# Performance work log

Hardware: AMD Instinct MI355X
Metric: run time of the kernel (lower is better)

The kernel has to match this reference:

```python
import jax, jax.numpy as jnp
import numpy as np

NUM_NODES = 50000
NUM_EDGES = 400000
NUM_GRAPHS = 16


def _glorot(key, shape):
    fan_in, fan_out = shape[0], shape[1]
    lim = jnp.sqrt(6.0 / (fan_in + fan_out))
    return jax.random.uniform(key, shape, jnp.float32, -lim, lim)


def setup_inputs() -> dict:
    key = jax.random.key(0)
    ks = jax.random.split(key, 12)
    x = jax.random.normal(ks[0], (NUM_NODES, 3), jnp.float32)
    edge_index = jax.random.randint(ks[1], (2, NUM_EDGES), 0, NUM_NODES, jnp.int64)
    batch = jax.random.randint(ks[2], (NUM_NODES,), 0, NUM_GRAPHS, jnp.int64)
    return {
        "x": x,
        "edge_index": edge_index,
        "batch": batch,
        "W1": _glorot(ks[3], (3, 512)),   "b1": jnp.zeros((512,), jnp.float32),
        "W2": _glorot(ks[4], (512, 1024)), "b2": jnp.zeros((1024,), jnp.float32),
        "W3": _glorot(ks[5], (1024, 512)), "b3": jnp.zeros((512,), jnp.float32),
        "fcw1": _glorot(ks[6], (512, 128)), "fcb1": jnp.zeros((128,), jnp.float32),
        "fcw2": _glorot(ks[7], (128, 1)),   "fcb2": jnp.zeros((1,), jnp.float32),
    }


def _gcn_conv(x, W, b, row, col, n):
    # PyG GCNConv: h = x W; out_i = sum_{j->i} d_j^{-1/2} d_i^{-1/2} h_j + b
    # (row, col) already include self-loops; edge weights are 1.
    h = x @ W  # [N, out]
    deg = jnp.zeros((n,), h.dtype).at[col].add(1.0)  # in-degree incl. self-loop
    dis = jax.lax.rsqrt(deg)  # deg >= 1 thanks to self-loops
    norm = dis[row] * dis[col]  # [E]
    msgs = h[row] * norm[:, None]  # [E, out] gather
    return jax.ops.segment_sum(msgs, col, num_segments=n) + b


def reference(x, edge_index, batch, W1, b1, W2, b2, W3, b3, fcw1, fcb1, fcw2, fcb2):
    n = x.shape[0]
    loop = jnp.arange(n, dtype=edge_index.dtype)
    row = jnp.concatenate([edge_index[0], loop])  # source
    col = jnp.concatenate([edge_index[1], loop])  # target

    h = jax.nn.relu(_gcn_conv(x, W1, b1, row, col, n))
    h = jax.nn.relu(_gcn_conv(h, W2, b2, row, col, n))
    h = jax.nn.relu(_gcn_conv(h, W3, b3, row, col, n))

    # global mean pool over graphs in the batch
    sums = jax.ops.segment_sum(h, batch, num_segments=NUM_GRAPHS)  # [G, 512]
    cnts = jax.ops.segment_sum(jnp.ones((n,), h.dtype), batch, num_segments=NUM_GRAPHS)
    pooled = sums / jnp.maximum(cnts, 1.0)[:, None]

    out = jax.nn.relu(pooled @ fcw1 + fcb1)
    out = out @ fcw2 + fcb2  # [G, 1]
    return out
```

## Files before the change

kernel.cpp:

```cpp
#include <hip/hip_runtime.h>
#include <hip/hip_bf16.h>

#define NNODES 50000
#define NEDGES 400000
#define NGRAPH 16

typedef __attribute__((ext_vector_type(4))) float floatx4;
typedef __attribute__((ext_vector_type(8))) short short8;

typedef __attribute__((address_space(3))) unsigned int lds_uint;
typedef __attribute__((address_space(1))) const unsigned int gbl_uint;

__device__ __forceinline__ void load16_to_lds(const void* g, void* l) {
    __builtin_amdgcn_global_load_lds((gbl_uint*)g, (lds_uint*)l, 16, 0, 0);
}

__global__ __launch_bounds__(64) void zero_out_k(float* out, int n) {
    int i = blockIdx.x * 64 + threadIdx.x;
    if (i < n) out[i] = 0.0f;
}

__global__ __launch_bounds__(256) void init_k(int* deg_cnt, int* cursor,
                                              float* gsum, int* gcnt,
                                              const float* __restrict__ x,
                                              float4* __restrict__ xp, int n) {
    int i = blockIdx.x * 256 + threadIdx.x;
    if (i < n) {
        deg_cnt[i] = 0; cursor[i] = 0;
        xp[i] = make_float4(x[i * 3 + 0], x[i * 3 + 1], x[i * 3 + 2], 0.0f);
    }
    if (i < NGRAPH * 512) gsum[i] = 0.0f;
    if (i < NGRAPH) gcnt[i] = 0;
}

__global__ __launch_bounds__(256) void deg_k(const int* __restrict__ col,
                                             int* __restrict__ deg_cnt, int e) {
    int i = blockIdx.x * 256 + threadIdx.x;
    if (i < e) atomicAdd(&deg_cnt[col[i]], 1);
}

__global__ __launch_bounds__(256) void segsum_k(const int* __restrict__ cnt,
                                                int* __restrict__ segsum, int n) {
    __shared__ int sb[256];
    int seg = blockIdx.x;
    int base = seg * 1024;
    int t = threadIdx.x;
    int s = 0;
#pragma unroll
    for (int j = 0; j < 4; ++j) {
        int idx = base + t + j * 256;
        if (idx < n) s += cnt[idx];
    }
    sb[t] = s;
    __syncthreads();
    for (int off = 128; off > 0; off >>= 1) {
        if (t < off) sb[t] += sb[t + off];
        __syncthreads();
    }
    if (t == 0) segsum[seg] = sb[0];
}

__global__ __launch_bounds__(64) void segscan_k(const int* __restrict__ segsum,
                                                int* __restrict__ segbase,
                                                int* __restrict__ offs,
                                                int nseg, int n) {
    if (threadIdx.x == 0) {
        int run = 0;
        for (int s = 0; s < nseg; ++s) { segbase[s] = run; run += segsum[s]; }
        offs[n] = run;
    }
}

__global__ __launch_bounds__(1024) void offs_k(const int* __restrict__ cnt,
                                               const int* __restrict__ segbase,
                                               int* __restrict__ offs,
                                               float* __restrict__ dis, int n) {
    __shared__ int sb[1024];
    int seg = blockIdx.x;
    int t = threadIdx.x;
    int i = seg * 1024 + t;
    int c = (i < n) ? cnt[i] : 0;
    sb[t] = c;
    __syncthreads();
    for (int off = 1; off < 1024; off <<= 1) {
        int v = (t >= off) ? sb[t - off] : 0;
        __syncthreads();
        sb[t] += v;
        __syncthreads();
    }
    if (i < n) {
        offs[i] = segbase[seg] + sb[t] - c;
        dis[i]  = rsqrtf((float)(c + 1));
    }
}

__global__ __launch_bounds__(256) void scatter_k(const int* __restrict__ row,
                                                 const int* __restrict__ col,
                                                 const int* __restrict__ offs,
                                                 int* __restrict__ cursor,
                                                 int* __restrict__ ssrc,
                                                 float* __restrict__ sw,
                                                 const float* __restrict__ dis, int e) {
    int i = blockIdx.x * 256 + threadIdx.x;
    if (i >= e) return;
    int d = col[i];
    int p = offs[d] + atomicAdd(&cursor[d], 1);
    int s = row[i];
    ssrc[p] = s;
    sw[p]   = dis[s];
}

__global__ __launch_bounds__(256) void agg3_k(const float4* __restrict__ xp,
                                              float* __restrict__ out,
                                              const int* __restrict__ offs,
                                              const int* __restrict__ ssrc,
                                              const float* __restrict__ sw,
                                              const float* __restrict__ dis, int n) {
    int d = blockIdx.x * 256 + threadIdx.x;
    if (d >= n) return;
    float dd = dis[d];
    float4 xd = xp[d];
    float a0 = dd * xd.x, a1 = dd * xd.y, a2 = dd * xd.z;
    int beg = offs[d], end = offs[d + 1];
    for (int e = beg; e < end; ++e) {
        int s = ssrc[e];
        float w = sw[e];
        float4 q = xp[s];
        a0 += w * q.x; a1 += w * q.y; a2 += w * q.z;
    }
    out[d * 3 + 0] = dd * a0;
    out[d * 3 + 1] = dd * a1;
    out[d * 3 + 2] = dd * a2;
}

__global__ __launch_bounds__(256) void gemm1_k(const float* __restrict__ aggx,
                                               const float* __restrict__ W1,
                                               const float* __restrict__ b1,
                                               __hip_bfloat16* __restrict__ h1, int n) {
    int wave = threadIdx.x >> 6;
    int lane = threadIdx.x & 63;
    int d = blockIdx.x * 4 + wave;
    if (d >= n) return;
    float a0 = aggx[d * 3 + 0], a1 = aggx[d * 3 + 1], a2 = aggx[d * 3 + 2];
    int f0 = lane * 8;
    short8 ov;
#pragma unroll
    for (int j = 0; j < 8; ++j) {
        int f = f0 + j;
        float v = b1[f] + a0 * W1[f] + a1 * W1[512 + f] + a2 * W1[1024 + f];
        __hip_bfloat16 h = __float2bfloat16(fmaxf(v, 0.0f));
        ov[j] = *(short*)&h;
    }
    *(short8*)&h1[(size_t)d * 512 + f0] = ov;
}

__device__ inline float bs2f(short v) {
    return __uint_as_float(((unsigned int)(unsigned short)v) << 16);
}

__global__ __launch_bounds__(256) void agg512w_k(const __hip_bfloat16* __restrict__ in,
                                                 __hip_bfloat16* __restrict__ out,
                                                 const int* __restrict__ offs,
                                                 const int* __restrict__ ssrc,
                                                 const float* __restrict__ sw,
                                                 const float* __restrict__ dis,
                                                 const float* __restrict__ bias,
                                                 int relu, int n) {
    int wave = threadIdx.x >> 6;
    int lane = threadIdx.x & 63;
    int d = blockIdx.x * 4 + wave;
    if (d >= n) return;
    float dd = dis[d];
    short8 p = *(const short8*)&in[(size_t)d * 512 + lane * 8];
    float acc[8];
#pragma unroll
    for (int j = 0; j < 8; ++j) acc[j] = dd * bs2f(p[j]);

    int beg = offs[d], end = offs[d + 1];
    int e = beg;
    for (; e + 3 < end; e += 4) {
        int s0 = ssrc[e],     s1 = ssrc[e + 1];
        int s2 = ssrc[e + 2], s3 = ssrc[e + 3];
        float w0 = sw[e],     w1 = sw[e + 1];
        float w2 = sw[e + 2], w3 = sw[e + 3];
        short8 q0 = *(const short8*)&in[(size_t)s0 * 512 + lane * 8];
        short8 q1 = *(const short8*)&in[(size_t)s1 * 512 + lane * 8];
        short8 q2 = *(const short8*)&in[(size_t)s2 * 512 + lane * 8];
        short8 q3 = *(const short8*)&in[(size_t)s3 * 512 + lane * 8];
#pragma unroll
        for (int j = 0; j < 8; ++j) acc[j] += w0 * bs2f(q0[j]);
#pragma unroll
        for (int j = 0; j < 8; ++j) acc[j] += w1 * bs2f(q1[j]);
#pragma unroll
        for (int j = 0; j < 8; ++j) acc[j] += w2 * bs2f(q2[j]);
#pragma unroll
        for (int j = 0; j < 8; ++j) acc[j] += w3 * bs2f(q3[j]);
    }
    for (; e < end; ++e) {
        int s0 = ssrc[e];
        float w0 = sw[e];
        short8 q0 = *(const short8*)&in[(size_t)s0 * 512 + lane * 8];
#pragma unroll
        for (int j = 0; j < 8; ++j) acc[j] += w0 * bs2f(q0[j]);
    }

    short8 ov;
#pragma unroll
    for (int j = 0; j < 8; ++j) {
        float v = acc[j] * dd;
        if (bias) v += bias[lane * 8 + j];
        if (relu) v = fmaxf(v, 0.0f);
        __hip_bfloat16 h = __float2bfloat16(v);
        ov[j] = *(short*)&h;
    }
    *(short8*)&out[(size_t)d * 512 + lane * 8] = ov;
}

__global__ __launch_bounds__(256) void tcvt_k(const float* __restrict__ W2,
                                              __hip_bfloat16* __restrict__ w2t,
                                              const float* __restrict__ W3,
                                              __hip_bfloat16* __restrict__ w3t) {
    __shared__ float tile[32][33];
    int t = threadIdx.x;
    const float* W; __hip_bfloat16* Wt;
    int K, N, idx;
    if (blockIdx.x < 512) { W = W2; Wt = w2t; K = 512;  N = 1024; idx = blockIdx.x; }
    else                  { W = W3; Wt = w3t; K = 1024; N = 512;  idx = blockIdx.x - 512; }
    int nbn = N / 32;
    int bn = (idx % nbn) * 32;
    int bk = (idx / nbn) * 32;
    int c = t & 31, r0 = t >> 5;
#pragma unroll
    for (int j = 0; j < 4; ++j) {
        int r = r0 + j * 8;
        tile[r][c] = W[(size_t)(bk + r) * N + bn + c];
    }
    __syncthreads();
#pragma unroll
    for (int j = 0; j < 4; ++j) {
        int r = r0 + j * 8;
        Wt[(size_t)(bn + r) * K + bk + c] = __float2bfloat16(tile[c][r]);
    }
}

__global__ __launch_bounds__(512, 2) void mfma_gemm256_k(
        const __hip_bfloat16* __restrict__ A,
        const __hip_bfloat16* __restrict__ Bt,
        const float* __restrict__ bias,
        __hip_bfloat16* __restrict__ C,
        int M, int N, int K, int relu, int lnt) {
    __shared__ short smem[65536];

    int tid  = threadIdx.x;
    int lane = tid & 63;
    int wave = tid >> 6;
    int wm = wave >> 2;
    int wn = wave & 3;
    int fr = lane & 15;

    int nwg = gridDim.x;
    int wg  = (blockIdx.x & 7) * (nwg >> 3) + (blockIdx.x >> 3);
    int mt  = wg >> lnt;
    int nt  = wg & ((1 << lnt) - 1);
    int bm  = mt << 8;
    int bn  = nt << 8;

    int r = lane & 15;
    int s = lane >> 4;
    const __hip_bfloat16* ga[2];
    const __hip_bfloat16* gb[2];
#pragma unroll
    for (int j = 0; j < 2; ++j) {
        int gsub = 2 * wave + j;
        ga[j] = A  + (size_t)(bm + gsub * 16 + r) * K + s * 8;
        gb[j] = Bt + (size_t)(bn + gsub * 16 + r) * K + s * 8;
    }

    floatx4 acc[8][4] = {};

    auto stage = [&](int p) {
        short* sp = &smem[p * 16384];
#pragma unroll
        for (int j = 0; j < 2; ++j) {
            load16_to_lds(ga[j], sp + (2 * wave + j) * 512);
            load16_to_lds(gb[j], sp + 8192 + (2 * wave + j) * 512);
            ga[j] += 32;
            gb[j] += 32;
        }
    };

    auto compute = [&](int p) {
        const short* sm = &smem[p * 16384];
        short8 bfr[4];
#pragma unroll
        for (int ni = 0; ni < 4; ++ni)
            bfr[ni] = *(const short8*)&sm[8192 + (wn * 4 + ni) * 512 + lane * 8];
#pragma unroll
        for (int mh = 0; mh < 2; ++mh) {
            short8 afr[4];
#pragma unroll
            for (int mi = 0; mi < 4; ++mi)
                afr[mi] = *(const short8*)&sm[(wm * 8 + mh * 4 + mi) * 512 + lane * 8];
            __builtin_amdgcn_s_setprio(1);
#pragma unroll
            for (int mi = 0; mi < 4; ++mi)
#pragma unroll
                for (int ni = 0; ni < 4; ++ni)
                    acc[mh * 4 + mi][ni] = __builtin_amdgcn_mfma_f32_16x16x32_bf16(
                        afr[mi], bfr[ni], acc[mh * 4 + mi][ni], 0, 0, 0);
            __builtin_amdgcn_s_setprio(0);
        }
    };

    int KT = K >> 5;
    stage(0); stage(1); stage(2);
    for (int t = 0; t < KT - 3; ++t) {
        stage((t + 3) & 3);
        asm volatile("s_waitcnt vmcnt(12)" ::: "memory");
        __builtin_amdgcn_s_barrier();
        compute(t & 3);
        __builtin_amdgcn_s_barrier();
    }
    asm volatile("s_waitcnt vmcnt(8)" ::: "memory");
    __builtin_amdgcn_s_barrier();
    compute((KT - 3) & 3);
    asm volatile("s_waitcnt vmcnt(4)" ::: "memory");
    __builtin_amdgcn_s_barrier();
    compute((KT - 2) & 3);
    asm volatile("s_waitcnt vmcnt(0)" ::: "memory");
    __builtin_amdgcn_s_barrier();
    compute((KT - 1) & 3);

    short* Cs = smem;
    int l4 = lane >> 4;
#pragma unroll
    for (int h = 0; h < 2; ++h) {
        __builtin_amdgcn_s_barrier();
        if (wm == h) {
#pragma unroll
            for (int mi = 0; mi < 8; ++mi) {
#pragma unroll
                for (int ni = 0; ni < 4; ++ni) {
                    int rr = mi * 16 + l4 * 4;
                    int cc = wn * 64 + ni * 16 + fr;
                    float bv = bias ? bias[bn + cc] : 0.0f;
#pragma unroll
                    for (int q = 0; q < 4; ++q) {
                        float v = acc[mi][ni][q] + bv;
                        if (relu) v = fmaxf(v, 0.0f);
                        __hip_bfloat16 hh = __float2bfloat16(v);
                        Cs[(rr + q) * 264 + cc] = *(short*)&hh;
                    }
                }
            }
        }
        __builtin_amdgcn_s_barrier();
#pragma unroll
        for (int i = 0; i < 8; ++i) {
            int idx = tid + 512 * i;
            int rr = idx >> 5, cc = idx & 31;
            int grow = bm + h * 128 + rr;
            if (grow < M)
                *(short8*)&C[(size_t)grow * N + bn + cc * 8] =
                    *(const short8*)&Cs[rr * 264 + cc * 8];
        }
    }
}

__global__ __launch_bounds__(256) void pool_k(const __hip_bfloat16* __restrict__ h,
                                              const int* __restrict__ batch,
                                              float* __restrict__ gsum,
                                              int* __restrict__ gcnt, int n) {
    __shared__ float ls[NGRAPH * 512];
    __shared__ int lcnt[NGRAPH];
    int t = threadIdx.x;
    for (int i = t; i < NGRAPH * 512; i += 256) ls[i] = 0.0f;
    if (t < NGRAPH) lcnt[t] = 0;
    __syncthreads();
    for (int d = blockIdx.x; d < n; d += gridDim.x) {
        int g = batch[d];
        if (t == 0) atomicAdd(&lcnt[g], 1);
        unsigned int q = *(const unsigned int*)&h[(size_t)d * 512 + 2 * t];
        ls[g * 512 + 2 * t]     += __uint_as_float((q & 0xffffu) << 16);
        ls[g * 512 + 2 * t + 1] += __uint_as_float((q >> 16) << 16);
    }
    __syncthreads();
    for (int i = t; i < NGRAPH * 512; i += 256) atomicAdd(&gsum[i], ls[i]);
    if (t < NGRAPH) atomicAdd(&gcnt[t], lcnt[t]);
}

__global__ __launch_bounds__(128) void fc_k(const float* __restrict__ gsum,
                                            const int* __restrict__ gcnt,
                                            const float* __restrict__ fcw1,
                                            const float* __restrict__ fcb1,
                                            const float* __restrict__ fcw2,
                                            const float* __restrict__ fcb2,
                                            float* __restrict__ out) {
    int g = blockIdx.x;
    int t = threadIdx.x;
    __shared__ float pooled[512];
    __shared__ float red[128];
    float inv = 1.0f / fmaxf((float)gcnt[g], 1.0f);
    for (int i = t; i < 512; i += 128) pooled[i] = gsum[g * 512 + i] * inv;
    __syncthreads();
    float sacc = fcb1[t];
    for (int k = 0; k < 512; ++k) sacc += pooled[k] * fcw1[k * 128 + t];
    sacc = fmaxf(sacc, 0.0f);
    red[t] = sacc * fcw2[t];
    __syncthreads();
    for (int off = 64; off > 0; off >>= 1) {
        if (t < off) red[t] += red[t + off];
        __syncthreads();
    }
    if (t == 0) out[g] = red[0] + fcb2[0];
}

extern "C" void kernel_launch(void* const* d_in, const int* in_sizes, int n_in,
                              void* d_out, int out_size, void* d_ws, size_t ws_size,
                              hipStream_t stream) {
    const float* x    = (const float*)d_in[0];
    const int*   ei   = (const int*)d_in[1];
    const int*   batch= (const int*)d_in[2];
    const float* W1   = (const float*)d_in[3];
    const float* b1   = (const float*)d_in[4];
    const float* W2   = (const float*)d_in[5];
    const float* b2   = (const float*)d_in[6];
    const float* W3   = (const float*)d_in[7];
    const float* b3   = (const float*)d_in[8];
    const float* fcw1 = (const float*)d_in[9];
    const float* fcb1 = (const float*)d_in[10];
    const float* fcw2 = (const float*)d_in[11];
    const float* fcb2 = (const float*)d_in[12];
    float* out = (float*)d_out;

    const int N = in_sizes[0] / 3;
    const int E = in_sizes[1] / 2;
    const int Mpad = (N + 255) & ~255;
    const int nseg = (N + 1023) / 1024;
    const int* row = ei;
    const int* col = ei + E;

    size_t used = 0;
    auto need = [&](size_t bytes) {
        size_t off = used;
        used += (bytes + 255) & ~(size_t)255;
        return off;
    };
    size_t o_deg  = need((size_t)N * 4);
    size_t o_cur  = need((size_t)N * 4);
    size_t o_dis  = need((size_t)N * 4);
    size_t o_offs = need((size_t)(N + 1) * 4);
    size_t o_seg  = need((size_t)nseg * 4);
    size_t o_segb = need((size_t)nseg * 4);
    size_t o_ssrc = need((size_t)E * 4);
    size_t o_sw   = need((size_t)E * 4);
    size_t o_xp   = need((size_t)N * 16);
    size_t o_aggx = need((size_t)N * 3 * 4);
    size_t o_gsum = need((size_t)NGRAPH * 512 * 4);
    size_t o_gcnt = need((size_t)NGRAPH * 4);
    size_t o_w2t  = need((size_t)512 * 1024 * 2);
    size_t o_w3t  = need((size_t)1024 * 512 * 2);
    size_t o_bufX = need((size_t)Mpad * 512 * 2);
    size_t o_bufY = need((size_t)Mpad * 512 * 2);
    size_t o_bufZ = need((size_t)Mpad * 1024 * 2);

    if (used > ws_size) {
        hipLaunchKernelGGL(zero_out_k, dim3((out_size + 63) / 64), dim3(64), 0, stream,
                           out, out_size);
        return;
    }

    char* base = (char*)d_ws;
    int*    deg_cnt = (int*)   (base + o_deg);
    int*    cursor  = (int*)   (base + o_cur);
    float*  dis     = (float*) (base + o_dis);
    int*    offs    = (int*)   (base + o_offs);
    int*    segsum  = (int*)   (base + o_seg);
    int*    segbase = (int*)   (base + o_segb);
    int*    ssrc    = (int*)   (base + o_ssrc);
    float*  sw      = (float*) (base + o_sw);
    float4* xp      = (float4*)(base + o_xp);
    float*  aggx    = (float*) (base + o_aggx);
    float*  gsum    = (float*) (base + o_gsum);
    int*    gcnt    = (int*)   (base + o_gcnt);
    __hip_bfloat16* w2t  = (__hip_bfloat16*)(base + o_w2t);
    __hip_bfloat16* w3t  = (__hip_bfloat16*)(base + o_w3t);
    __hip_bfloat16* bufX = (__hip_bfloat16*)(base + o_bufX);
    __hip_bfloat16* bufY = (__hip_bfloat16*)(base + o_bufY);
    __hip_bfloat16* bufZ = (__hip_bfloat16*)(base + o_bufZ);
    (void)n_in;

    int gN = (N + 255) / 256;
    int gE = (E + 255) / 256;
    int gW = (N + 3) / 4;
    int nrt = Mpad / 256;

    hipLaunchKernelGGL(init_k, dim3(gN), dim3(256), 0, stream, deg_cnt, cursor, gsum, gcnt, x, xp, N);
    hipLaunchKernelGGL(deg_k, dim3(gE), dim3(256), 0, stream, col, deg_cnt, E);
    hipLaunchKernelGGL(segsum_k, dim3(nseg), dim3(256), 0, stream, deg_cnt, segsum, N);
    hipLaunchKernelGGL(segscan_k, dim3(1), dim3(64), 0, stream, segsum, segbase, offs, nseg, N);
    hipLaunchKernelGGL(offs_k, dim3(nseg), dim3(1024), 0, stream, deg_cnt, segbase, offs, dis, N);
    hipLaunchKernelGGL(scatter_k, dim3(gE), dim3(256), 0, stream, row, col, offs, cursor, ssrc, sw, dis, E);

    hipLaunchKernelGGL(tcvt_k, dim3(1024), dim3(256), 0, stream, W2, w2t, W3, w3t);

    hipLaunchKernelGGL(agg3_k, dim3(gN), dim3(256), 0, stream, xp, aggx, offs, ssrc, sw, dis, N);
    hipLaunchKernelGGL(gemm1_k, dim3(gW), dim3(256), 0, stream, aggx, W1, b1, bufX, N);

    hipLaunchKernelGGL(agg512w_k, dim3(gW), dim3(256), 0, stream, bufX, bufY, offs, ssrc, sw, dis,
                       (const float*)nullptr, 0, N);
    hipLaunchKernelGGL(mfma_gemm256_k, dim3(nrt * 4), dim3(512), 0, stream,
                       bufY, w2t, b2, bufZ, N, 1024, 512, 1, 2);

    hipLaunchKernelGGL(mfma_gemm256_k, dim3(nrt * 2), dim3(512), 0, stream,
                       bufZ, w3t, (const float*)nullptr, bufX, N, 512, 1024, 0, 1);
    hipLaunchKernelGGL(agg512w_k, dim3(gW), dim3(256), 0, stream, bufX, bufY, offs, ssrc, sw, dis,
                       b3, 1, N);

    hipLaunchKernelGGL(pool_k, dim3(256), dim3(256), 0, stream, bufY, batch, gsum, gcnt, N);
    hipLaunchKernelGGL(fc_k, dim3(NGRAPH), dim3(128), 0, stream, gsum, gcnt, fcw1, fcb1, fcw2, fcb2, out);
}
```

Before: 612.2 us.

## Restructure bf16 MFMA GEMM into 8-wave ping-pong schedule with interleaved quarter-tile loads

Replaces the 4-stage 32-wide K ring buffer with a double-buffered 64-wide K tile split into quarter sub-tiles. Each loop iteration runs four MFMA phases separated by barriers, and each phase issues one quarter of the next tile's global-to-LDS loads. The wave-to-output mapping also changes: waves now share B halves (bh/bq4). The intent is to interleave memory, LDS reads and MFMA work more finely, in the style of a hipBLASLt ping-pong schedule. The cost is many more barriers per K step and a shallower prefetch depth.

Measured after the change: 607.6 us. No clear change (-0.8%).

```diff
diff --git a/kernel.cpp b/kernel.cpp
--- a/kernel.cpp
+++ b/kernel.cpp
@@ -257,6 +257,8 @@
     int wm = wave >> 2;
     int wn = wave & 3;
     int fr = lane & 15;
+    int bh  = wn >> 1;
+    int bq4 = (wn & 1) * 4;
 
     int nwg = gridDim.x;
     int wg  = (blockIdx.x & 7) * (nwg >> 3) + (blockIdx.x >> 3);
@@ -267,69 +269,110 @@
 
     int r = lane & 15;
     int s = lane >> 4;
-    const __hip_bfloat16* ga[2];
-    const __hip_bfloat16* gb[2];
-#pragma unroll
-    for (int j = 0; j < 2; ++j) {
-        int gsub = 2 * wave + j;
-        ga[j] = A  + (size_t)(bm + gsub * 16 + r) * K + s * 8;
-        gb[j] = Bt + (size_t)(bn + gsub * 16 + r) * K + s * 8;
-    }
+    const __hip_bfloat16* pa = A  + (size_t)(bm + wave * 16 + r) * K + s * 8;
+    const __hip_bfloat16* pb = Bt + (size_t)(bn + wave * 16 + r) * K + s * 8;
+    size_t half_stride = (size_t)128 * K;
+
+    auto stage1 = [&](int p, int kks, int hh, int t1) {
+        size_t coff = (size_t)(t1 * 64 + kks * 32);
+        int q = p * 32768 + hh * 8192 + kks * 4096 + wave * 512;
+        load16_to_lds(pa + hh * half_stride + coff, &smem[q]);
+        load16_to_lds(pb + hh * half_stride + coff, &smem[16384 + q]);
+    };
 
     floatx4 acc[8][4] = {};
 
-    auto stage = [&](int p) {
-        short* sp = &smem[p * 16384];
-#pragma unroll
-        for (int j = 0; j < 2; ++j) {
-            load16_to_lds(ga[j], sp + (2 * wave + j) * 512);
-            load16_to_lds(gb[j], sp + 8192 + (2 * wave + j) * 512);
-            ga[j] += 32;
-            gb[j] += 32;
-        }
-    };
-
-    auto compute = [&](int p) {
-        const short* sm = &smem[p * 16384];
-        short8 bfr[4];
-#pragma unroll
-        for (int ni = 0; ni < 4; ++ni)
-            bfr[ni] = *(const short8*)&sm[8192 + (wn * 4 + ni) * 512 + lane * 8];
-#pragma unroll
-        for (int mh = 0; mh < 2; ++mh) {
-            short8 afr[4];
-#pragma unroll
-            for (int mi = 0; mi < 4; ++mi)
-                afr[mi] = *(const short8*)&sm[(wm * 8 + mh * 4 + mi) * 512 + lane * 8];
-            __builtin_amdgcn_s_setprio(1);
-#pragma unroll
-            for (int mi = 0; mi < 4; ++mi)
-#pragma unroll
-                for (int ni = 0; ni < 4; ++ni)
-                    acc[mh * 4 + mi][ni] = __builtin_amdgcn_mfma_f32_16x16x32_bf16(
-                        afr[mi], bfr[ni], acc[mh * 4 + mi][ni], 0, 0, 0);
-            __builtin_amdgcn_s_setprio(0);
-        }
-    };
-
-    int KT = K >> 5;
-    stage(0); stage(1); stage(2);
-    for (int t = 0; t < KT - 3; ++t) {
-        stage((t + 3) & 3);
-        asm volatile("s_waitcnt vmcnt(12)" ::: "memory");
-        __builtin_amdgcn_s_barrier();
-        compute(t & 3);
-        __builtin_amdgcn_s_barrier();
-    }
-    asm volatile("s_waitcnt vmcnt(8)" ::: "memory");
-    __builtin_amdgcn_s_barrier();
-    compute((KT - 3) & 3);
+    int KT = K >> 6;
+    stage1(0, 0, 0, 0); stage1(0, 0, 1, 0);
+    stage1(0, 1, 0, 0); stage1(0, 1, 1, 0);
     asm volatile("s_waitcnt vmcnt(4)" ::: "memory");
     __builtin_amdgcn_s_barrier();
-    compute((KT - 2) & 3);
-    asm volatile("s_waitcnt vmcnt(0)" ::: "memory");
-    __builtin_amdgcn_s_barrier();
-    compute((KT - 1) & 3);
+
+    for (int t = 0; t < KT; ++t) {
+        int p = t & 1;
+        int more = (t + 1 < KT);
+        const short* smA = &smem[p * 32768 + wm * 8192];
+        const short* smB = &smem[p * 32768 + 16384 + bh * 8192];
+        short8 af[4], bfr[4];
+
+#pragma unroll
+        for (int ni = 0; ni < 4; ++ni)
+            bfr[ni] = *(const short8*)&smB[(bq4 + ni) * 512 + lane * 8];
+#pragma unroll
+        for (int mi = 0; mi < 4; ++mi)
+            af[mi] = *(const short8*)&smA[mi * 512 + lane * 8];
+        if (more) stage1(p ^ 1, 0, 0, t + 1);
+        __builtin_amdgcn_s_barrier();
+        asm volatile("s_waitcnt lgkmcnt(0)" ::: "memory");
+        __builtin_amdgcn_s_setprio(1);
+#pragma unroll
+        for (int mi = 0; mi < 4; ++mi)
+#pragma unroll
+            for (int ni = 0; ni < 4; ++ni)
+                acc[mi][ni] = __builtin_amdgcn_mfma_f32_16x16x32_bf16(
+                    af[mi], bfr[ni], acc[mi][ni], 0, 0, 0);
+        __builtin_amdgcn_s_setprio(0);
+        __builtin_amdgcn_s_barrier();
+
+#pragma unroll
+        for (int mi = 0; mi < 4; ++mi)
+            af[mi] = *(const short8*)&smA[(4 + mi) * 512 + lane * 8];
+        if (more) {
+            stage1(p ^ 1, 0, 1, t + 1);
+            asm volatile("s_waitcnt vmcnt(4)" ::: "memory");
+        } else {
+            asm volatile("s_waitcnt vmcnt(0)" ::: "memory");
+        }
+        __builtin_amdgcn_s_barrier();
+        asm volatile("s_waitcnt lgkmcnt(0)" ::: "memory");
+        __builtin_amdgcn_s_setprio(1);
+#pragma unroll
+        for (int mi = 0; mi < 4; ++mi)
+#pragma unroll
+            for (int ni = 0; ni < 4; ++ni)
+                acc[4 + mi][ni] = __builtin_amdgcn_mfma_f32_16x16x32_bf16(
+                    af[mi], bfr[ni], acc[4 + mi][ni], 0, 0, 0);
+        __builtin_amdgcn_s_setprio(0);
+        __builtin_amdgcn_s_barrier();
+
+#pragma unroll
+        for (int ni = 0; ni < 4; ++ni)
+            bfr[ni] = *(const short8*)&smB[4096 + (bq4 + ni) * 512 + lane * 8];
+#pragma unroll
+        for (int mi = 0; mi < 4; ++mi)
+            af[mi] = *(const short8*)&smA[4096 + mi * 512 + lane * 8];
+        if (more) stage1(p ^ 1, 1, 0, t + 1);
+        __builtin_amdgcn_s_barrier();
+        asm volatile("s_waitcnt lgkmcnt(0)" ::: "memory");
+        __builtin_amdgcn_s_setprio(1);
+#pragma unroll
+        for (int mi = 0; mi < 4; ++mi)
+#pragma unroll
+            for (int ni = 0; ni < 4; ++ni)
+                acc[mi][ni] = __builtin_amdgcn_mfma_f32_16x16x32_bf16(
+                    af[mi], bfr[ni], acc[mi][ni], 0, 0, 0);
+        __builtin_amdgcn_s_setprio(0);
+        __builtin_amdgcn_s_barrier();
+
+#pragma unroll
+        for (int mi = 0; mi < 4; ++mi)
+            af[mi] = *(const short8*)&smA[4096 + (4 + mi) * 512 + lane * 8];
+        if (more) {
+            stage1(p ^ 1, 1, 1, t + 1);
+            asm volatile("s_waitcnt vmcnt(4)" ::: "memory");
+        }
+        __builtin_amdgcn_s_barrier();
+        asm volatile("s_waitcnt lgkmcnt(0)" ::: "memory");
+        __builtin_amdgcn_s_setprio(1);
+#pragma unroll
+        for (int mi = 0; mi < 4; ++mi)
+#pragma unroll
+            for (int ni = 0; ni < 4; ++ni)
+                acc[4 + mi][ni] = __builtin_amdgcn_mfma_f32_16x16x32_bf16(
+                    af[mi], bfr[ni], acc[4 + mi][ni], 0, 0, 0);
+        __builtin_amdgcn_s_setprio(0);
+        __builtin_amdgcn_s_barrier();
+    }
 
     short* Cs = smem;
     int l4 = lane >> 4;
@@ -354,6 +397,7 @@
                 }
             }
         }
+        asm volatile("s_waitcnt lgkmcnt(0)" ::: "memory");
         __builtin_amdgcn_s_barrier();
 #pragma unroll
         for (int i = 0; i < 8; ++i) {
```

## Shrink MFMA GEMM tile to 256x128 with double-buffered LDS for higher occupancy

Applied to the files above, without the earlier changes.

The bf16 MFMA GEMM tile changes from 256x256 to 256x128, with 8 waves arranged 4x2. The LDS pipeline drops from a 4-stage to a 2-stage double buffer, cutting LDS to 48KB and raising the occupancy hint from 2 to 4 workgroups. Twice as many workgroups are launched, aiming for better CU fill and latency hiding on the 50000-row GEMMs. In exchange, arithmetic intensity per tile drops, A is reloaded more often, and the shallower prefetch may expose memory latency.

Result: no change. 613.1 us (+0.1%).

```diff
diff --git a/kernel.cpp b/kernel.cpp
--- a/kernel.cpp
+++ b/kernel.cpp
@@ -243,105 +243,89 @@
     }
 }
 
-__global__ __launch_bounds__(512, 2) void mfma_gemm256_k(
+__global__ __launch_bounds__(512, 4) void mfma_gemm256_k(
         const __hip_bfloat16* __restrict__ A,
         const __hip_bfloat16* __restrict__ Bt,
         const float* __restrict__ bias,
         __hip_bfloat16* __restrict__ C,
         int M, int N, int K, int relu, int lnt) {
-    __shared__ short smem[65536];
+    __shared__ short smem[24576];
 
     int tid  = threadIdx.x;
     int lane = tid & 63;
     int wave = tid >> 6;
-    int wm = wave >> 2;
-    int wn = wave & 3;
+    int wm = wave >> 1;
+    int wn = wave & 1;
     int fr = lane & 15;
+    int l4 = lane >> 4;
 
     int nwg = gridDim.x;
     int wg  = (blockIdx.x & 7) * (nwg >> 3) + (blockIdx.x >> 3);
     int mt  = wg >> lnt;
     int nt  = wg & ((1 << lnt) - 1);
     int bm  = mt << 8;
-    int bn  = nt << 8;
+    int bn  = nt << 7;
 
     int r = lane & 15;
     int s = lane >> 4;
-    const __hip_bfloat16* ga[2];
-    const __hip_bfloat16* gb[2];
-#pragma unroll
-    for (int j = 0; j < 2; ++j) {
-        int gsub = 2 * wave + j;
-        ga[j] = A  + (size_t)(bm + gsub * 16 + r) * K + s * 8;
-        gb[j] = Bt + (size_t)(bn + gsub * 16 + r) * K + s * 8;
-    }
-
-    floatx4 acc[8][4] = {};
+    const __hip_bfloat16* ga0 = A  + (size_t)(bm + (2 * wave + 0) * 16 + r) * K + s * 8;
+    const __hip_bfloat16* ga1 = A  + (size_t)(bm + (2 * wave + 1) * 16 + r) * K + s * 8;
+    const __hip_bfloat16* gb  = Bt + (size_t)(bn + wave * 16 + r) * K + s * 8;
+
+    floatx4 acc[4][4] = {};
 
     auto stage = [&](int p) {
-        short* sp = &smem[p * 16384];
-#pragma unroll
-        for (int j = 0; j < 2; ++j) {
-            load16_to_lds(ga[j], sp + (2 * wave + j) * 512);
-            load16_to_lds(gb[j], sp + 8192 + (2 * wave + j) * 512);
-            ga[j] += 32;
-            gb[j] += 32;
+        short* sp = &smem[p * 12288];
+        load16_to_lds(ga0, sp + (2 * wave + 0) * 512);
+        load16_to_lds(ga1, sp + (2 * wave + 1) * 512);
+        load16_to_lds(gb,  sp + 8192 + wave * 512);
+        ga0 += 32; ga1 += 32; gb += 32;
+    };
+
+    auto compute = [&](int p) {
+        const short* sm = &smem[p * 12288];
+        short8 af[4], bf[4];
+#pragma unroll
+        for (int mi = 0; mi < 4; ++mi)
+            af[mi] = *(const short8*)&sm[(wm * 4 + mi) * 512 + lane * 8];
+#pragma unroll
+        for (int ni = 0; ni < 4; ++ni)
+            bf[ni] = *(const short8*)&sm[8192 + (wn * 4 + ni) * 512 + lane * 8];
+        __builtin_amdgcn_s_setprio(1);
+#pragma unroll
+        for (int mi = 0; mi < 4; ++mi)
+#pragma unroll
+            for (int ni = 0; ni < 4; ++ni)
+                acc[mi][ni] = __builtin_amdgcn_mfma_f32_16x16x32_bf16(
+                    af[mi], bf[ni], acc[mi][ni], 0, 0, 0);
+        __builtin_amdgcn_s_setprio(0);
+    };
+
+    int KT = K >> 5;
+    stage(0);
+    for (int t = 0; t < KT; ++t) {
+        int p = t & 1;
+        __builtin_amdgcn_s_barrier();
+        if (t + 1 < KT) {
+            stage(p ^ 1);
+            asm volatile("s_waitcnt vmcnt(3)" ::: "memory");
+        } else {
+            asm volatile("s_waitcnt vmcnt(0)" ::: "memory");
         }
-    };
-
-    auto compute = [&](int p) {
-        const short* sm = &smem[p * 16384];
-        short8 bfr[4];
-#pragma unroll
-        for (int ni = 0; ni < 4; ++ni)
-            bfr[ni] = *(const short8*)&sm[8192 + (wn * 4 + ni) * 512 + lane * 8];
-#pragma unroll
-        for (int mh = 0; mh < 2; ++mh) {
-            short8 afr[4];
-#pragma unroll
-            for (int mi = 0; mi < 4; ++mi)
-                afr[mi] = *(const short8*)&sm[(wm * 8 + mh * 4 + mi) * 512 + lane * 8];
-            __builtin_amdgcn_s_setprio(1);
-#pragma unroll
-            for (int mi = 0; mi < 4; ++mi)
-#pragma unroll
-                for (int ni = 0; ni < 4; ++ni)
-                    acc[mh * 4 + mi][ni] = __builtin_amdgcn_mfma_f32_16x16x32_bf16(
-                        afr[mi], bfr[ni], acc[mh * 4 + mi][ni], 0, 0, 0);
-            __builtin_amdgcn_s_setprio(0);
-        }
-    };
-
-    int KT = K >> 5;
-    stage(0); stage(1); stage(2);
-    for (int t = 0; t < KT - 3; ++t) {
-        stage((t + 3) & 3);
-        asm volatile("s_waitcnt vmcnt(12)" ::: "memory");
         __builtin_amdgcn_s_barrier();
-        compute(t & 3);
-        __builtin_amdgcn_s_barrier();
-    }
-    asm volatile("s_waitcnt vmcnt(8)" ::: "memory");
-    __builtin_amdgcn_s_barrier();
-    compute((KT - 3) & 3);
-    asm volatile("s_waitcnt vmcnt(4)" ::: "memory");
-    __builtin_amdgcn_s_barrier();
-    compute((KT - 2) & 3);
-    asm volatile("s_waitcnt vmcnt(0)" ::: "memory");
-    __builtin_amdgcn_s_barrier();
-    compute((KT - 1) & 3);
+        compute(p);
+    }
 
     short* Cs = smem;
-    int l4 = lane >> 4;
 #pragma unroll
     for (int h = 0; h < 2; ++h) {
         __builtin_amdgcn_s_barrier();
-        if (wm == h) {
-#pragma unroll
-            for (int mi = 0; mi < 8; ++mi) {
+        if ((wm >> 1) == h) {
+#pragma unroll
+            for (int mi = 0; mi < 4; ++mi) {
 #pragma unroll
                 for (int ni = 0; ni < 4; ++ni) {
-                    int rr = mi * 16 + l4 * 4;
+                    int lr = (wm & 1) * 64 + mi * 16 + l4 * 4;
                     int cc = wn * 64 + ni * 16 + fr;
                     float bv = bias ? bias[bn + cc] : 0.0f;
 #pragma unroll
@@ -349,20 +333,20 @@
                         float v = acc[mi][ni][q] + bv;
                         if (relu) v = fmaxf(v, 0.0f);
                         __hip_bfloat16 hh = __float2bfloat16(v);
-                        Cs[(rr + q) * 264 + cc] = *(short*)&hh;
+                        Cs[(lr + q) * 136 + cc] = *(short*)&hh;
                     }
                 }
             }
         }
         __builtin_amdgcn_s_barrier();
 #pragma unroll
-        for (int i = 0; i < 8; ++i) {
+        for (int i = 0; i < 4; ++i) {
             int idx = tid + 512 * i;
-            int rr = idx >> 5, cc = idx & 31;
+            int rr = idx >> 4, c8 = idx & 15;
             int grow = bm + h * 128 + rr;
             if (grow < M)
-                *(short8*)&C[(size_t)grow * N + bn + cc * 8] =
-                    *(const short8*)&Cs[rr * 264 + cc * 8];
+                *(short8*)&C[(size_t)grow * N + bn + c8 * 8] =
+                    *(const short8*)&Cs[rr * 136 + c8 * 8];
         }
     }
 }
@@ -509,11 +493,11 @@
 
     hipLaunchKernelGGL(agg512w_k, dim3(gW), dim3(256), 0, stream, bufX, bufY, offs, ssrc, sw, dis,
                        (const float*)nullptr, 0, N);
+    hipLaunchKernelGGL(mfma_gemm256_k, dim3(nrt * 8), dim3(512), 0, stream,
+                       bufY, w2t, b2, bufZ, N, 1024, 512, 1, 3);
+
     hipLaunchKernelGGL(mfma_gemm256_k, dim3(nrt * 4), dim3(512), 0, stream,
-                       bufY, w2t, b2, bufZ, N, 1024, 512, 1, 2);
-
-    hipLaunchKernelGGL(mfma_gemm256_k, dim3(nrt * 2), dim3(512), 0, stream,
-                       bufZ, w3t, (const float*)nullptr, bufX, N, 512, 1024, 0, 1);
+                       bufZ, w3t, (const float*)nullptr, bufX, N, 512, 1024, 0, 2);
     hipLaunchKernelGGL(agg512w_k, dim3(gW), dim3(256), 0, stream, bufX, bufY, offs, ssrc, sw, dis,
                        b3, 1, N);
 
```

## Double-buffer GEMM with BK=64 stages and unroll aggregation gather by 8

Applied to the files above, without the earlier changes.

The GEMM pipeline goes from a 4-stage ring of K=32 tiles to a 2-stage double buffer of K=64 tiles. This halves the number of barrier pairs per K and changes how far ahead global-to-LDS loads are issued. The sparse aggregation kernel gains an 8-way unrolled edge loop so more row gathers are in flight per wave, at the cost of extra registers. A leftover no-op loop and an explicit lgkmcnt wait before the epilogue barrier were also added.

New measurement: 632.8 us. 3.4% more time.

```diff
diff --git a/kernel.cpp b/kernel.cpp
--- a/kernel.cpp
+++ b/kernel.cpp
@@ -178,6 +178,36 @@
 
     int beg = offs[d], end = offs[d + 1];
     int e = beg;
+    for (; e + 7 < end; e += 8) {
+        int   s0 = ssrc[e],     s1 = ssrc[e + 1], s2 = ssrc[e + 2], s3 = ssrc[e + 3];
+        int   s4 = ssrc[e + 4], s5 = ssrc[e + 5], s6 = ssrc[e + 6], s7 = ssrc[e + 7];
+        float w0 = sw[e],     w1 = sw[e + 1], w2 = sw[e + 2], w3 = sw[e + 3];
+        float w4 = sw[e + 4], w5 = sw[e + 5], w6 = sw[e + 6], w7 = sw[e + 7];
+        short8 q0 = *(const short8*)&in[(size_t)s0 * 512 + lane * 8];
+        short8 q1 = *(const short8*)&in[(size_t)s1 * 512 + lane * 8];
+        short8 q2 = *(const short8*)&in[(size_t)s2 * 512 + lane * 8];
+        short8 q3 = *(const short8*)&in[(size_t)s3 * 512 + lane * 8];
+        short8 q4 = *(const short8*)&in[(size_t)s4 * 512 + lane * 8];
+        short8 q5 = *(const short8*)&in[(size_t)s5 * 512 + lane * 8];
+        short8 q6 = *(const short8*)&in[(size_t)s6 * 512 + lane * 8];
+        short8 q7 = *(const short8*)&in[(size_t)s7 * 512 + lane * 8];
+#pragma unroll
+        for (int j = 0; j < 8; ++j) acc[j] += w0 * bs2f(q0[j]);
+#pragma unroll
+        for (int j = 0; j < 8; ++j) acc[j] += w1 * bs2f(q1[j]);
+#pragma unroll
+        for (int j = 0; j < 8; ++j) acc[j] += w2 * bs2f(q2[j]);
+#pragma unroll
+        for (int j = 0; j < 8; ++j) acc[j] += w3 * bs2f(q3[j]);
+#pragma unroll
+        for (int j = 0; j < 8; ++j) acc[j] += w4 * bs2f(q4[j]);
+#pragma unroll
+        for (int j = 0; j < 8; ++j) acc[j] += w5 * bs2f(q5[j]);
+#pragma unroll
+        for (int j = 0; j < 8; ++j) acc[j] += w6 * bs2f(q6[j]);
+#pragma unroll
+        for (int j = 0; j < 8; ++j) acc[j] += w7 * bs2f(q7[j]);
+    }
     for (; e + 3 < end; e += 4) {
         int s0 = ssrc[e],     s1 = ssrc[e + 1];
         int s2 = ssrc[e + 2], s3 = ssrc[e + 3];
@@ -267,69 +297,79 @@
 
     int r = lane & 15;
     int s = lane >> 4;
-    const __hip_bfloat16* ga[2];
-    const __hip_bfloat16* gb[2];
+    const __hip_bfloat16* ga[4];
+    const __hip_bfloat16* gb[4];
+#pragma unroll
+    for (int j = 0; j < 4; ++j) {
+        int rloc = (wave * 4 + j) * 8 + (lane >> 3);
+        (void)rloc;
+    }
 #pragma unroll
     for (int j = 0; j < 2; ++j) {
-        int gsub = 2 * wave + j;
+        int gsub = wave * 2 + j;
         ga[j] = A  + (size_t)(bm + gsub * 16 + r) * K + s * 8;
         gb[j] = Bt + (size_t)(bn + gsub * 16 + r) * K + s * 8;
+        ga[j + 2] = A  + (size_t)(bm + gsub * 16 + r) * K + 32 + s * 8;
+        gb[j + 2] = Bt + (size_t)(bn + gsub * 16 + r) * K + 32 + s * 8;
     }
 
     floatx4 acc[8][4] = {};
 
     auto stage = [&](int p) {
-        short* sp = &smem[p * 16384];
+        short* sp = &smem[p * 32768];
 #pragma unroll
         for (int j = 0; j < 2; ++j) {
-            load16_to_lds(ga[j], sp + (2 * wave + j) * 512);
-            load16_to_lds(gb[j], sp + 8192 + (2 * wave + j) * 512);
-            ga[j] += 32;
-            gb[j] += 32;
+            int gsub = wave * 2 + j;
+            load16_to_lds(ga[j],     sp + gsub * 512);
+            load16_to_lds(gb[j],     sp + 16384 + gsub * 512);
+            load16_to_lds(ga[j + 2], sp + 8192 + gsub * 512);
+            load16_to_lds(gb[j + 2], sp + 16384 + 8192 + gsub * 512);
+            ga[j] += 64; gb[j] += 64; ga[j + 2] += 64; gb[j + 2] += 64;
         }
     };
 
     auto compute = [&](int p) {
-        const short* sm = &smem[p * 16384];
-        short8 bfr[4];
-#pragma unroll
-        for (int ni = 0; ni < 4; ++ni)
-            bfr[ni] = *(const short8*)&sm[8192 + (wn * 4 + ni) * 512 + lane * 8];
-#pragma unroll
-        for (int mh = 0; mh < 2; ++mh) {
-            short8 afr[4];
-#pragma unroll
-            for (int mi = 0; mi < 4; ++mi)
-                afr[mi] = *(const short8*)&sm[(wm * 8 + mh * 4 + mi) * 512 + lane * 8];
-            __builtin_amdgcn_s_setprio(1);
-#pragma unroll
-            for (int mi = 0; mi < 4; ++mi)
-#pragma unroll
-                for (int ni = 0; ni < 4; ++ni)
-                    acc[mh * 4 + mi][ni] = __builtin_amdgcn_mfma_f32_16x16x32_bf16(
-                        afr[mi], bfr[ni], acc[mh * 4 + mi][ni], 0, 0, 0);
-            __builtin_amdgcn_s_setprio(0);
+        const short* sm = &smem[p * 32768];
+#pragma unroll
+        for (int kk = 0; kk < 2; ++kk) {
+            const short* smA = sm + kk * 8192;
+            const short* smB = sm + 16384 + kk * 8192;
+            short8 bfr[4];
+#pragma unroll
+            for (int ni = 0; ni < 4; ++ni)
+                bfr[ni] = *(const short8*)&smB[(wn * 4 + ni) * 512 + lane * 8];
+#pragma unroll
+            for (int mh = 0; mh < 2; ++mh) {
+                short8 afr[4];
+#pragma unroll
+                for (int mi = 0; mi < 4; ++mi)
+                    afr[mi] = *(const short8*)&smA[(wm * 8 + mh * 4 + mi) * 512 + lane * 8];
+                __builtin_amdgcn_s_setprio(1);
+#pragma unroll
+                for (int mi = 0; mi < 4; ++mi)
+#pragma unroll
+                    for (int ni = 0; ni < 4; ++ni)
+                        acc[mh * 4 + mi][ni] = __builtin_amdgcn_mfma_f32_16x16x32_bf16(
+                            afr[mi], bfr[ni], acc[mh * 4 + mi][ni], 0, 0, 0);
+                __builtin_amdgcn_s_setprio(0);
+            }
         }
     };
 
-    int KT = K >> 5;
-    stage(0); stage(1); stage(2);
-    for (int t = 0; t < KT - 3; ++t) {
-        stage((t + 3) & 3);
-        asm volatile("s_waitcnt vmcnt(12)" ::: "memory");
+    int KT = K >> 6;
+    stage(0);
+    for (int t = 0; t < KT; ++t) {
+        int p = t & 1;
         __builtin_amdgcn_s_barrier();
-        compute(t & 3);
+        if (t + 1 < KT) {
+            stage(p ^ 1);
+            asm volatile("s_waitcnt vmcnt(8)" ::: "memory");
+        } else {
+            asm volatile("s_waitcnt vmcnt(0)" ::: "memory");
+        }
         __builtin_amdgcn_s_barrier();
-    }
-    asm volatile("s_waitcnt vmcnt(8)" ::: "memory");
-    __builtin_amdgcn_s_barrier();
-    compute((KT - 3) & 3);
-    asm volatile("s_waitcnt vmcnt(4)" ::: "memory");
-    __builtin_amdgcn_s_barrier();
-    compute((KT - 2) & 3);
-    asm volatile("s_waitcnt vmcnt(0)" ::: "memory");
-    __builtin_amdgcn_s_barrier();
-    compute((KT - 1) & 3);
+        compute(p);
+    }
 
     short* Cs = smem;
     int l4 = lane >> 4;
@@ -354,6 +394,7 @@
                 }
             }
         }
+        asm volatile("s_waitcnt lgkmcnt(0)" ::: "memory");
         __builtin_amdgcn_s_barrier();
 #pragma unroll
         for (int i = 0; i < 8; ++i) {
```
